# Performance work log

Hardware: AMD Instinct MI355X
Metric: run time of the kernel (lower is better)

Reference implementation:

```python
import jax, jax.numpy as jnp
import numpy as np

DIM = 1024
N_HEADS = 16
HEAD_DIM = DIM // N_HEADS
MLP_DIM = 4096
B, L, M = 4, 1024, 1024
EPS = 1e-5


def _mha(q_in, k_in, v_in, mask, wq, wk, wv, wo):
    b, l, d = q_in.shape
    m = k_in.shape[1]
    # torch view(b, l, head_dim, n_heads): split last dim as (head_dim, n_heads)
    q = (q_in @ wq).reshape(b, l, HEAD_DIM, N_HEADS)
    k = (k_in @ wk).reshape(b, m, HEAD_DIM, N_HEADS)
    v = (v_in @ wv).reshape(b, m, HEAD_DIM, N_HEADS)  # computed but unused downstream (source quirk)
    score = jnp.einsum('bldn,bmdn->blmn', q, k)
    # source applies mask BEFORE scaling
    score = jnp.where(mask, jnp.float32(-1e9), score)
    score = score / (HEAD_DIM ** 0.5)
    attn = jax.nn.softmax(score, axis=2)
    # SOURCE QUIRK: second einsum uses k, not v — reproduced faithfully
    x = jnp.einsum('blmn,bmdn->bldn', attn, k)
    x = x.reshape(b, l, d)  # 'b l d n -> b l (d n)'
    return x @ wo


def _layer_norm(x, g, b):
    mu = jnp.mean(x, axis=-1, keepdims=True)
    var = jnp.var(x, axis=-1, keepdims=True)
    return (x - mu) * jax.lax.rsqrt(var + EPS) * g + b


def setup_inputs() -> dict:
    key = jax.random.key(0)
    ks = jax.random.split(key, 16)
    s = 0.02
    inp = {
        'x': jax.random.normal(ks[0], (B, L, DIM), dtype=jnp.float32),
        'enc_output': jax.random.normal(ks[1], (B, M, DIM), dtype=jnp.float32),
        # causal mask: True above diagonal => masked
        'self_attn_mask': jnp.triu(jnp.ones((L, L), dtype=bool), k=1)[None, :, :, None],
        'enc_dec_mask': jnp.zeros((1, L, M, 1), dtype=bool),
        'sa_wq': s * jax.random.normal(ks[2], (DIM, DIM), jnp.float32),
        'sa_wk': s * jax.random.normal(ks[3], (DIM, DIM), jnp.float32),
        'sa_wv': s * jax.random.normal(ks[4], (DIM, DIM), jnp.float32),
        'sa_wo': s * jax.random.normal(ks[5], (DIM, DIM), jnp.float32),
        'ca_wq': s * jax.random.normal(ks[6], (DIM, DIM), jnp.float32),
        'ca_wk': s * jax.random.normal(ks[7], (DIM, DIM), jnp.float32),
        'ca_wv': s * jax.random.normal(ks[8], (DIM, DIM), jnp.float32),
        'ca_wo': s * jax.random.normal(ks[9], (DIM, DIM), jnp.float32),
        'ln1_g': jnp.ones((DIM,), jnp.float32), 'ln1_b': jnp.zeros((DIM,), jnp.float32),
        'ln2_g': jnp.ones((DIM,), jnp.float32), 'ln2_b': jnp.zeros((DIM,), jnp.float32),
        'ln3_g': jnp.ones((DIM,), jnp.float32), 'ln3_b': jnp.zeros((DIM,), jnp.float32),
        'ff_w1': s * jax.random.normal(ks[10], (DIM, MLP_DIM), jnp.float32),
        'ff_b1': jnp.zeros((MLP_DIM,), jnp.float32),
        'ff_w2': s * jax.random.normal(ks[11], (MLP_DIM, DIM), jnp.float32),
        'ff_b2': jnp.zeros((DIM,), jnp.float32),
    }
    return inp


def reference(x, enc_output, self_attn_mask, enc_dec_mask,
              sa_wq, sa_wk, sa_wv, sa_wo,
              ca_wq, ca_wk, ca_wv, ca_wo,
              ln1_g, ln1_b, ln2_g, ln2_b, ln3_g, ln3_b,
              ff_w1, ff_b1, ff_w2, ff_b2):
    # self-attention + residual + LN (dropout = identity in eval)
    h = x + _mha(x, x, x, self_attn_mask, sa_wq, sa_wk, sa_wv, sa_wo)
    h = _layer_norm(h, ln1_g, ln1_b)
    # encoder-decoder attention + residual + LN
    h = h + _mha(h, enc_output, enc_output, enc_dec_mask, ca_wq, ca_wk, ca_wv, ca_wo)
    h = _layer_norm(h, ln2_g, ln2_b)
    # position-wise FFN (gelu, exact erf like torch default) + residual + LN
    ff = jax.nn.gelu(h @ ff_w1 + ff_b1, approximate=False) @ ff_w2 + ff_b2
    h = h + ff
    h = _layer_norm(h, ln3_g, ln3_b)
    return h
```

## Files before the change

### kernel.cpp

```cpp
#include <hip/hip_runtime.h>
#include <hip/hip_bf16.h>
#include <stdint.h>

typedef unsigned short u16;
typedef _Float16 f16x8 __attribute__((ext_vector_type(8)));
typedef float f32x4 __attribute__((ext_vector_type(4)));

#define TOK 4096

__device__ __forceinline__ u16 f2h(float f) {
  _Float16 h = (_Float16)f;
  return __builtin_bit_cast(unsigned short, h);
}
__device__ __forceinline__ unsigned pack2(float a, float b) {
  return (unsigned)f2h(a) | ((unsigned)f2h(b) << 16);
}
__device__ __forceinline__ void gld16(const u16* g, u16* l) {
  __builtin_amdgcn_global_load_lds(
      (const __attribute__((address_space(1))) void*)g,
      (__attribute__((address_space(3))) void*)l, 16, 0, 0);
}
__device__ __forceinline__ float gelu_fast(float v) {
  float z = 1.5957691216f * v * (1.0f + 0.044715f * v * v);
  return v / (1.0f + __expf(-z));
}

__global__ __launch_bounds__(256) void cast_f16_kernel(const float* __restrict__ in,
                                                       u16* __restrict__ out, int n8) {
  int i = blockIdx.x * 256 + threadIdx.x;
  if (i >= n8) return;
  const float4* p = (const float4*)(in + (size_t)i * 8);
  float4 a = p[0], b = p[1];
  uint4 o;
  o.x = pack2(a.x, a.y); o.y = pack2(a.z, a.w);
  o.z = pack2(b.x, b.y); o.w = pack2(b.z, b.w);
  *(uint4*)(out + (size_t)i * 8) = o;
}

__device__ __forceinline__ void tc_body(const float* W, u16* Wt, int K, int N,
                                        int bx, int by, int tid) {
  __shared__ float tile[32][33];
  int n0 = bx * 32, k0 = by * 32;
  int tx = tid & 31, ty = tid >> 5;
#pragma unroll
  for (int e = 0; e < 4; e++)
    tile[ty + e * 8][tx] = W[(size_t)(k0 + ty + e * 8) * N + n0 + tx];
  __syncthreads();
#pragma unroll
  for (int e = 0; e < 4; e++)
    Wt[(size_t)(n0 + ty + e * 8) * K + k0 + tx] = f2h(tile[tx][ty + e * 8]);
}
__global__ __launch_bounds__(256) void transpose_cast_kernel(const float* __restrict__ W,
                                                             u16* __restrict__ Wt,
                                                             int K, int N) {
  tc_body(W, Wt, K, N, blockIdx.x, blockIdx.y, threadIdx.x);
}
__global__ __launch_bounds__(256) void transpose_cast6_kernel(
    const float* W0, const float* W1, const float* W2,
    const float* W3, const float* W4, const float* W5,
    u16* T0, u16* T1, u16* T2, u16* T3, u16* T4, u16* T5) {
  const float* W; u16* T;
  switch (blockIdx.z) {
    case 0: W = W0; T = T0; break;
    case 1: W = W1; T = T1; break;
    case 2: W = W2; T = T2; break;
    case 3: W = W3; T = T3; break;
    case 4: W = W4; T = T4; break;
    default: W = W5; T = T5; break;
  }
  tc_body(W, T, 1024, 1024, blockIdx.x, blockIdx.y, threadIdx.x);
}

template <int EPI, int BN>
__global__ __launch_bounds__((BN == 256) ? 512 : 256)
void gemm_bt_kernel(const u16* __restrict__ A0,
                    const u16* __restrict__ A1,
                    const u16* __restrict__ Bt0,
                    const u16* __restrict__ Bt1,
                    float* __restrict__ Cf,
                    u16* __restrict__ Cb0,
                    u16* __restrict__ Cb1,
                    u16* __restrict__ CbT,
                    const float* __restrict__ bias,
                    int M, int N, int K, int KLEN) {
  const u16* A  = (EPI == 0 && blockIdx.z) ? A1 : A0;
  const u16* Bt = (EPI == 0 && blockIdx.z) ? Bt1 : Bt0;
  u16* Cb = (EPI == 0 && blockIdx.z) ? Cb1 : Cb0;
  __shared__ u16 As[2][128 * 32];
  __shared__ u16 Bs[2][BN * 32];
  int tid = threadIdx.x, lane = tid & 63, wid = tid >> 6;
  int gx = gridDim.x, gy = gridDim.y;
  int nwg = gx * gy;
  int flat = blockIdx.x + gx * blockIdx.y;
  int k8 = flat & 7, idx = flat >> 3;
  int bx, by;
  if (gx >= 16) {
    int rx = gx >> 2, ry = gy >> 1;
    int kx = k8 & 3, ky = k8 >> 2;
    bx = kx * rx + idx % rx;
    by = ky * ry + idx / rx;
  } else {
    int widx = k8 * (nwg >> 3) + idx;
    bx = widx % gx;
    by = widx / gx;
  }
  int row0 = by * 128, col0 = bx * BN;
  int wm = (BN == 256) ? (wid >> 2) * 64 : (wid >> 1) * 64;
  int wn = (BN == 256) ? (wid & 3) * 64 : (wid & 1) * 64;
  int sr = tid >> 2;
  int scol = (((tid & 3) ^ (sr & 3)) * 8);
  size_t koff = (EPI == 4) ? (size_t)blockIdx.z * KLEN : 0;
  const u16* Ab0 = A + (size_t)(row0 + sr) * K + koff + scol;
  const u16* Ab1 = A + (size_t)(row0 + 64 + sr) * K + koff + scol;
  const u16* Bb0 = Bt + (size_t)(col0 + sr) * K + koff + scol;
  const u16* Bb1 = Bt + (size_t)(col0 + ((BN == 256) ? 128 : 64) + sr) * K + koff + scol;
  f32x4 acc[4][4];
#pragma unroll
  for (int i = 0; i < 4; i++)
#pragma unroll
    for (int j = 0; j < 4; j++) { acc[i][j][0] = 0.f; acc[i][j][1] = 0.f; acc[i][j][2] = 0.f; acc[i][j][3] = 0.f; }
  int KT = KLEN >> 5;
  int ra = lane & 15, kg = lane >> 4;
  int aoff[4], boff[4];
#pragma unroll
  for (int i = 0; i < 4; i++) {
    int r = wm + i * 16 + ra;
    aoff[i] = r * 32 + ((kg ^ (r & 3)) * 8);
    int c = wn + i * 16 + ra;
    boff[i] = c * 32 + ((kg ^ (c & 3)) * 8);
  }

  auto STAGE = [&](int kt, int buf) {
    if constexpr (BN == 256) {
      gld16(Ab0 + kt * 32, &As[buf][wid * 512]);
      gld16(Bb0 + kt * 32, &Bs[buf][wid * 512]);
      gld16(Bb1 + kt * 32, &Bs[buf][4096 + wid * 512]);
    } else {
      gld16(Ab0 + kt * 32, &As[buf][wid * 512]);
      gld16(Ab1 + kt * 32, &As[buf][2048 + wid * 512]);
      gld16(Bb0 + kt * 32, &Bs[buf][wid * 512]);
      gld16(Bb1 + kt * 32, &Bs[buf][2048 + wid * 512]);
    }
  };

  STAGE(0, 0);
  __syncthreads();
  int cur = 0;
  for (int kt = 0; kt < KT; ++kt) {
    if (kt + 1 < KT) STAGE(kt + 1, cur ^ 1);
    f16x8 af[4], bfv[4];
#pragma unroll
    for (int i = 0; i < 4; i++) af[i] = *(const f16x8*)&As[cur][aoff[i]];
#pragma unroll
    for (int j = 0; j < 4; j++) bfv[j] = *(const f16x8*)&Bs[cur][boff[j]];
#pragma unroll
    for (int i = 0; i < 4; i++)
#pragma unroll
      for (int j = 0; j < 4; j++)
        acc[i][j] = __builtin_amdgcn_mfma_f32_16x16x32_f16(af[i], bfv[j], acc[i][j], 0, 0, 0);
    __syncthreads();
    cur ^= 1;
  }

  int rq = kg * 4;
#pragma unroll
  for (int i = 0; i < 4; i++) {
    int rowb = row0 + wm + i * 16 + rq;
    if (EPI == 0) {
      int b = rowb >> 10, l0 = rowb & 1023;
      int d0 = (col0 + wn) >> 4;
      size_t hb = ((size_t)(b * 16 + ra)) * 1024;
      u16 h[4][4];
#pragma unroll
      for (int j = 0; j < 4; j++)
#pragma unroll
        for (int q = 0; q < 4; q++) h[j][q] = f2h(acc[i][j][q]);
#pragma unroll
      for (int q = 0; q < 4; q++) {
        ushort4 hv;
        hv.x = h[0][q]; hv.y = h[1][q]; hv.z = h[2][q]; hv.w = h[3][q];
        *(ushort4*)&Cb[(hb + l0 + q) * 64 + d0] = hv;
      }
      if (blockIdx.z) {
#pragma unroll
        for (int j = 0; j < 4; j++) {
          uint2 ov;
          ov.x = (unsigned)h[j][0] | ((unsigned)h[j][1] << 16);
          ov.y = (unsigned)h[j][2] | ((unsigned)h[j][3] << 16);
          *(uint2*)&CbT[(hb >> 10 << 16) + ((size_t)(d0 + j)) * 1024 + l0] = ov;
        }
      }
    } else {
#pragma unroll
      for (int j = 0; j < 4; j++) {
        int col = col0 + wn + j * 16 + ra;
        float bval = 0.f;
        if (EPI == 2) bval = bias[col];
        if (EPI == 4 && blockIdx.z == 0 && bias) bval = bias[col];
#pragma unroll
        for (int q = 0; q < 4; q++) {
          int row = rowb + q;
          float v = acc[i][j][q] + bval;
          if (EPI == 2) {
            Cb[(size_t)row * N + col] = f2h(gelu_fast(v));
          } else {
            Cf[(size_t)blockIdx.z * M * N + (size_t)row * N + col] = v;
          }
        }
      }
    }
  }
}

template <bool CAUSAL>
__global__ __launch_bounds__(256) void flash3_kernel(const u16* __restrict__ Qh,
                                                     const u16* __restrict__ Kh,
                                                     const u16* __restrict__ KhT,
                                                     u16* __restrict__ Xtok) {
  const int L = 1024;
  int tid = threadIdx.x, lane = tid & 63, wid = tid >> 6;
  int gx = gridDim.x, nwg = gx * gridDim.y;
  int flat = blockIdx.x + gx * blockIdx.y;
  int widx = (flat & 7) * (nwg >> 3) + (flat >> 3);
  int qt = widx % gx, bh = widx / gx;
  if (CAUSAL) qt = gx - 1 - qt;
  __shared__ u16 Ks[2][4096];
  __shared__ u16 Kt[2][4096];
  __shared__ u16 Ps[4][2048];
  int ra = lane & 15, kg = lane >> 4;
  int rq = kg * 4;
  int wr0 = qt * 128 + wid * 32;
  f16x8 qa[2][2];
#pragma unroll
  for (int i = 0; i < 2; i++) {
    const u16* Qb = Qh + ((size_t)bh * L + wr0 + i * 16 + ra) * 64;
    qa[i][0] = *(const f16x8*)(Qb + kg * 8);
    qa[i][1] = *(const f16x8*)(Qb + 32 + kg * 8);
  }
  f32x4 oacc[2][4];
#pragma unroll
  for (int i = 0; i < 2; i++)
#pragma unroll
    for (int d = 0; d < 4; d++) { oacc[i][d][0] = 0.f; oacc[i][d][1] = 0.f; oacc[i][d][2] = 0.f; oacc[i][d][3] = 0.f; }
  float l_i[2][4];
#pragma unroll
  for (int i = 0; i < 2; i++)
#pragma unroll
    for (int q = 0; q < 4; q++) l_i[i][q] = 0.f;
  int ntiles = CAUSAL ? (2 * qt + 2) : 16;
  int fr = lane >> 3, fc = lane & 7;

#define KSTAGE(mt, buf) do {                                                        \
    {                                                                               \
      int rr = wid * 8 + fr;                                                        \
      int cc = fc ^ fr;                                                             \
      gld16(Kh + ((size_t)bh * L + (mt) * 64 + rr) * 64 + cc * 8, &Ks[buf][wid * 512]);          \
      gld16(KhT + ((size_t)bh * 64 + rr) * L + (size_t)(mt) * 64 + cc * 8, &Kt[buf][wid * 512]); \
    }                                                                               \
    {                                                                               \
      int rr = 32 + wid * 8 + fr;                                                   \
      int cc = fc ^ fr;                                                             \
      gld16(Kh + ((size_t)bh * L + (mt) * 64 + rr) * 64 + cc * 8, &Ks[buf][2048 + wid * 512]);          \
      gld16(KhT + ((size_t)bh * 64 + rr) * L + (size_t)(mt) * 64 + cc * 8, &Kt[buf][2048 + wid * 512]); \
    }                                                                               \
  } while (0)

  KSTAGE(0, 0);
  __syncthreads();
  int cur = 0;
  for (int mt = 0; mt < ntiles; ++mt) {
    if (mt + 1 < ntiles) KSTAGE(mt + 1, cur ^ 1);
    bool active = !(CAUSAL && (wr0 + 31 < mt * 64));
    if (active) {
      bool wmask = CAUSAL && (mt * 64 + 63 > wr0);
      float p[2][4][4];
      __builtin_amdgcn_s_setprio(1);
#pragma unroll
      for (int j = 0; j < 4; j++) {
        int krow = j * 16 + ra;
        int s2 = krow & 7;
        f16x8 kb0 = *(const f16x8*)&Ks[cur][krow * 64 + ((kg ^ s2) * 8)];
        f16x8 kb1 = *(const f16x8*)&Ks[cur][krow * 64 + (((4 + kg) ^ s2) * 8)];
#pragma unroll
        for (int i = 0; i < 2; i++) {
          f32x4 a; a[0] = 0.f; a[1] = 0.f; a[2] = 0.f; a[3] = 0.f;
          a = __builtin_amdgcn_mfma_f32_16x16x32_f16(qa[i][0], kb0, a, 0, 0, 0);
          a = __builtin_amdgcn_mfma_f32_16x16x32_f16(qa[i][1], kb1, a, 0, 0, 0);
#pragma unroll
          for (int q = 0; q < 4; q++) {
            float v = a[q] * 0.125f;
            if (wmask) {
              int rg = wr0 + i * 16 + rq + q;
              int cg = mt * 64 + j * 16 + ra;
              if (cg > rg) v = -1.25e8f;
            }
            p[i][j][q] = __expf(v);
          }
        }
      }
      __builtin_amdgcn_s_setprio(0);
#pragma unroll
      for (int i = 0; i < 2; i++) {
        float rs[4] = {0.f, 0.f, 0.f, 0.f};
#pragma unroll
        for (int j = 0; j < 4; j++)
#pragma unroll
          for (int q = 0; q < 4; q++) rs[q] += p[i][j][q];
#pragma unroll
        for (int off = 1; off < 16; off <<= 1)
#pragma unroll
          for (int q = 0; q < 4; q++) rs[q] += __shfl_xor(rs[q], off);
#pragma unroll
        for (int q = 0; q < 4; q++) l_i[i][q] += rs[q];
      }
#pragma unroll
      for (int i = 0; i < 2; i++)
#pragma unroll
        for (int j = 0; j < 4; j++)
#pragma unroll
          for (int q = 0; q < 4; q++) {
            int prow = i * 16 + rq + q;
            int pcol = j * 16 + ra;
            Ps[wid][prow * 64 + (((pcol >> 3) ^ (prow & 7)) * 8) + (pcol & 7)] = f2h(p[i][j][q]);
          }
      f16x8 pa[2][2];
#pragma unroll
      for (int i = 0; i < 2; i++) {
        int arow = i * 16 + ra;
        int s3 = arow & 7;
        pa[i][0] = *(const f16x8*)&Ps[wid][arow * 64 + ((kg ^ s3) * 8)];
        pa[i][1] = *(const f16x8*)&Ps[wid][arow * 64 + (((4 + kg) ^ s3) * 8)];
      }
      __builtin_amdgcn_s_setprio(1);
#pragma unroll
      for (int d = 0; d < 4; d++) {
        int krow = d * 16 + ra;
        int s4 = krow & 7;
        f16x8 kc0 = *(const f16x8*)&Kt[cur][krow * 64 + ((kg ^ s4) * 8)];
        f16x8 kc1 = *(const f16x8*)&Kt[cur][krow * 64 + (((4 + kg) ^ s4) * 8)];
#pragma unroll
        for (int i = 0; i < 2; i++) {
          oacc[i][d] = __builtin_amdgcn_mfma_f32_16x16x32_f16(pa[i][0], kc0, oacc[i][d], 0, 0, 0);
          oacc[i][d] = __builtin_amdgcn_mfma_f32_16x16x32_f16(pa[i][1], kc1, oacc[i][d], 0, 0, 0);
        }
      }
      __builtin_amdgcn_s_setprio(0);
    }
    __syncthreads();
    cur ^= 1;
  }
#undef KSTAGE
  int b = bh >> 4, nh = bh & 15;
#pragma unroll
  for (int i = 0; i < 2; i++)
#pragma unroll
    for (int q = 0; q < 4; q++) {
      float inv = 1.0f / l_i[i][q];
      int l = wr0 + i * 16 + rq + q;
      size_t rowg = ((size_t)b * 1024 + l) * 1024;
#pragma unroll
      for (int d = 0; d < 4; d++)
        Xtok[rowg + (d * 16 + ra) * 16 + nh] = f2h(oacc[i][d][q] * inv);
    }
}

template <int WRITE_H, int TWO>
__global__ __launch_bounds__(256) void ln_kernel(const float* __restrict__ a,
                                                 const float* __restrict__ a2,
                                                 const float* __restrict__ res,
                                                 const float* __restrict__ g,
                                                 const float* __restrict__ bb,
                                                 float* __restrict__ outf,
                                                 u16* __restrict__ outh) {
  int row = blockIdx.x, tid = threadIdx.x;
  int lane = tid & 63, wid = tid >> 6;
  size_t base = (size_t)row * 1024 + tid * 4;
  float4 va = *(const float4*)(a + base);
  float4 vr = *(const float4*)(res + base);
  float x0 = va.x + vr.x, x1 = va.y + vr.y, x2 = va.z + vr.z, x3 = va.w + vr.w;
  if (TWO) {
    float4 v2 = *(const float4*)(a2 + base);
    x0 += v2.x; x1 += v2.y; x2 += v2.z; x3 += v2.w;
  }
  float s = x0 + x1 + x2 + x3;
  float sq = x0 * x0 + x1 * x1 + x2 * x2 + x3 * x3;
#pragma unroll
  for (int off = 1; off < 64; off <<= 1) {
    s += __shfl_xor(s, off);
    sq += __shfl_xor(sq, off);
  }
  __shared__ float red[8];
  if (lane == 0) { red[wid] = s; red[4 + wid] = sq; }
  __syncthreads();
  s = red[0] + red[1] + red[2] + red[3];
  sq = red[4] + red[5] + red[6] + red[7];
  float mean = s * (1.0f / 1024.0f);
  float var = sq * (1.0f / 1024.0f) - mean * mean;
  float rstd = rsqrtf(var + 1e-5f);
  float4 vg = *(const float4*)(g + tid * 4);
  float4 vb = *(const float4*)(bb + tid * 4);
  float y0 = (x0 - mean) * rstd * vg.x + vb.x;
  float y1 = (x1 - mean) * rstd * vg.y + vb.y;
  float y2 = (x2 - mean) * rstd * vg.z + vb.z;
  float y3 = (x3 - mean) * rstd * vg.w + vb.w;
  float4 yo; yo.x = y0; yo.y = y1; yo.z = y2; yo.w = y3;
  *(float4*)(outf + base) = yo;
  if (WRITE_H) {
    uint2 ov; ov.x = pack2(y0, y1); ov.y = pack2(y2, y3);
    *(uint2*)(outh + base) = ov;
  }
}

extern "C" void kernel_launch(void* const* d_in, const int* in_sizes, int n_in,
                              void* d_out, int out_size, void* d_ws, size_t ws_size,
                              hipStream_t stream) {
  (void)in_sizes; (void)n_in; (void)out_size; (void)ws_size;
  const float* x    = (const float*)d_in[0];
  const float* enc  = (const float*)d_in[1];
  const float* sa_wq = (const float*)d_in[4];
  const float* sa_wk = (const float*)d_in[5];
  const float* sa_wo = (const float*)d_in[7];
  const float* ca_wq = (const float*)d_in[8];
  const float* ca_wk = (const float*)d_in[9];
  const float* ca_wo = (const float*)d_in[11];
  const float* ln1g = (const float*)d_in[12];
  const float* ln1b = (const float*)d_in[13];
  const float* ln2g = (const float*)d_in[14];
  const float* ln2b = (const float*)d_in[15];
  const float* ln3g = (const float*)d_in[16];
  const float* ln3b = (const float*)d_in[17];
  const float* ffw1 = (const float*)d_in[18];
  const float* ffb1 = (const float*)d_in[19];
  const float* ffw2 = (const float*)d_in[20];
  const float* ffb2 = (const float*)d_in[21];

  uint8_t* w = (uint8_t*)d_ws;
  const size_t MB = 1024ull * 1024ull;
  u16* wt_saq = (u16*)(w + 0 * MB);
  u16* wt_sak = (u16*)(w + 2 * MB);
  u16* wt_sao = (u16*)(w + 4 * MB);
  u16* wt_caq = (u16*)(w + 6 * MB);
  u16* wt_cak = (u16*)(w + 8 * MB);
  u16* wt_cao = (u16*)(w + 10 * MB);
  u16* wt_ff1 = (u16*)(w + 12 * MB);
  u16* wt_ff2 = (u16*)(w + 20 * MB);
  u16* act_h  = (u16*)(w + 28 * MB);
  u16* enc_h  = (u16*)(w + 36 * MB);
  u16* qhd    = (u16*)(w + 44 * MB);
  u16* khd    = (u16*)(w + 52 * MB);
  u16* khdT   = (u16*)(w + 60 * MB);
  u16* ctxtok = (u16*)(w + 68 * MB);
  float* Cf32 = (float*)(w + 76 * MB);
  float* hA   = (float*)(w + 108 * MB);
  float* hB   = (float*)(w + 124 * MB);
  u16* ff1h = qhd;
  float* Cf32b = Cf32 + 4194304;

  cast_f16_kernel<<<2048, 256, 0, stream>>>(x, act_h, 524288);
  cast_f16_kernel<<<2048, 256, 0, stream>>>(enc, enc_h, 524288);
  transpose_cast6_kernel<<<dim3(32, 32, 6), 256, 0, stream>>>(
      sa_wq, sa_wk, sa_wo, ca_wq, ca_wk, ca_wo,
      wt_saq, wt_sak, wt_sao, wt_caq, wt_cak, wt_cao);
  transpose_cast_kernel<<<dim3(128, 32), 256, 0, stream>>>(ffw1, wt_ff1, 1024, 4096);
  transpose_cast_kernel<<<dim3(32, 128), 256, 0, stream>>>(ffw2, wt_ff2, 4096, 1024);

  gemm_bt_kernel<0, 128><<<dim3(8, 32, 2), 256, 0, stream>>>(
      act_h, act_h, wt_saq, wt_sak, nullptr, qhd, khd, khdT, nullptr, TOK, 1024, 1024, 1024);
  flash3_kernel<true><<<dim3(8, 64), 256, 0, stream>>>(qhd, khd, khdT, ctxtok);
  gemm_bt_kernel<4, 128><<<dim3(8, 32, 2), 256, 0, stream>>>(
      ctxtok, ctxtok, wt_sao, wt_sao, Cf32, nullptr, nullptr, nullptr, nullptr, TOK, 1024, 1024, 512);
  ln_kernel<1, 1><<<4096, 256, 0, stream>>>(Cf32, Cf32b, x, ln1g, ln1b, hA, act_h);

  gemm_bt_kernel<0, 128><<<dim3(8, 32, 2), 256, 0, stream>>>(
      act_h, enc_h, wt_caq, wt_cak, nullptr, qhd, khd, khdT, nullptr, TOK, 1024, 1024, 1024);
  flash3_kernel<false><<<dim3(8, 64), 256, 0, stream>>>(qhd, khd, khdT, ctxtok);
  gemm_bt_kernel<4, 128><<<dim3(8, 32, 2), 256, 0, stream>>>(
      ctxtok, ctxtok, wt_cao, wt_cao, Cf32, nullptr, nullptr, nullptr, nullptr, TOK, 1024, 1024, 512);
  ln_kernel<1, 1><<<4096, 256, 0, stream>>>(Cf32, Cf32b, hA, ln2g, ln2b, hB, act_h);

  gemm_bt_kernel<2, 256><<<dim3(16, 32, 1), 512, 0, stream>>>(
      act_h, act_h, wt_ff1, wt_ff1, nullptr, ff1h, ff1h, nullptr, ffb1, TOK, 4096, 1024, 1024);
  gemm_bt_kernel<4, 128><<<dim3(8, 32, 2), 256, 0, stream>>>(
      ff1h, ff1h, wt_ff2, wt_ff2, Cf32, nullptr, nullptr, nullptr, ffb2, TOK, 1024, 4096, 2048);
  ln_kernel<0, 1><<<4096, 256, 0, stream>>>(Cf32, Cf32b, hB, ln3g, ln3b, (float*)d_out, nullptr);
}
```

Baseline: 370.3 us.

## Store split-K partials in fp16, fuse prep kernels, widen FF2 split-K to four

The split-K GEMM partial outputs are now written as fp16 instead of fp32, and the layer-norm kernel sums a template number of fp16 partials with the residual. This halves partial-sum traffic. The FF2 GEMM moves from two to four K splits for more parallelism. All input casts and weight transposes are merged into one launch. Rounding each partial to fp16 loses some accuracy before the residual add.

After: 362.9 us. 2.0% less time.

```diff
diff --git a/kernel.cpp b/kernel.cpp
--- a/kernel.cpp
+++ b/kernel.cpp
@@ -11,6 +11,9 @@
 __device__ __forceinline__ u16 f2h(float f) {
   _Float16 h = (_Float16)f;
   return __builtin_bit_cast(unsigned short, h);
+}
+__device__ __forceinline__ float h2f(u16 b) {
+  return (float)__builtin_bit_cast(_Float16, b);
 }
 __device__ __forceinline__ unsigned pack2(float a, float b) {
   return (unsigned)f2h(a) | ((unsigned)f2h(b) << 16);
@@ -25,10 +28,21 @@
   return v / (1.0f + __expf(-z));
 }
 
-__global__ __launch_bounds__(256) void cast_f16_kernel(const float* __restrict__ in,
-                                                       u16* __restrict__ out, int n8) {
-  int i = blockIdx.x * 256 + threadIdx.x;
-  if (i >= n8) return;
+__device__ __forceinline__ void tc_body(const float* W, u16* Wt, int K, int N,
+                                        int bx, int by, int tid) {
+  __shared__ float tile[32][33];
+  int n0 = bx * 32, k0 = by * 32;
+  int tx = tid & 31, ty = tid >> 5;
+#pragma unroll
+  for (int e = 0; e < 4; e++)
+    tile[ty + e * 8][tx] = W[(size_t)(k0 + ty + e * 8) * N + n0 + tx];
+  __syncthreads();
+#pragma unroll
+  for (int e = 0; e < 4; e++)
+    Wt[(size_t)(n0 + ty + e * 8) * K + k0 + tx] = f2h(tile[tx][ty + e * 8]);
+}
+__device__ __forceinline__ void cast_body(const float* in, u16* out, int blk, int tid) {
+  int i = blk * 256 + tid;
   const float4* p = (const float4*)(in + (size_t)i * 8);
   float4 a = p[0], b = p[1];
   uint4 o;
@@ -37,38 +51,39 @@
   *(uint4*)(out + (size_t)i * 8) = o;
 }
 
-__device__ __forceinline__ void tc_body(const float* W, u16* Wt, int K, int N,
-                                        int bx, int by, int tid) {
-  __shared__ float tile[32][33];
-  int n0 = bx * 32, k0 = by * 32;
-  int tx = tid & 31, ty = tid >> 5;
-#pragma unroll
-  for (int e = 0; e < 4; e++)
-    tile[ty + e * 8][tx] = W[(size_t)(k0 + ty + e * 8) * N + n0 + tx];
-  __syncthreads();
-#pragma unroll
-  for (int e = 0; e < 4; e++)
-    Wt[(size_t)(n0 + ty + e * 8) * K + k0 + tx] = f2h(tile[tx][ty + e * 8]);
-}
-__global__ __launch_bounds__(256) void transpose_cast_kernel(const float* __restrict__ W,
-                                                             u16* __restrict__ Wt,
-                                                             int K, int N) {
-  tc_body(W, Wt, K, N, blockIdx.x, blockIdx.y, threadIdx.x);
-}
-__global__ __launch_bounds__(256) void transpose_cast6_kernel(
+__global__ __launch_bounds__(256) void prep_kernel(
+    const float* x, const float* enc, u16* xh, u16* ench,
     const float* W0, const float* W1, const float* W2,
     const float* W3, const float* W4, const float* W5,
-    u16* T0, u16* T1, u16* T2, u16* T3, u16* T4, u16* T5) {
-  const float* W; u16* T;
-  switch (blockIdx.z) {
-    case 0: W = W0; T = T0; break;
-    case 1: W = W1; T = T1; break;
-    case 2: W = W2; T = T2; break;
-    case 3: W = W3; T = T3; break;
-    case 4: W = W4; T = T4; break;
-    default: W = W5; T = T5; break;
-  }
-  tc_body(W, T, 1024, 1024, blockIdx.x, blockIdx.y, threadIdx.x);
+    u16* T0, u16* T1, u16* T2, u16* T3, u16* T4, u16* T5,
+    const float* Wff1, u16* Tff1, const float* Wff2, u16* Tff2) {
+  int blk = blockIdx.x, tid = threadIdx.x;
+  if (blk < 2048) { cast_body(x, xh, blk, tid); return; }
+  if (blk < 4096) { cast_body(enc, ench, blk - 2048, tid); return; }
+  if (blk < 10240) {
+    int t = blk - 4096;
+    int z = t >> 10, s = t & 1023;
+    const float* W; u16* T;
+    switch (z) {
+      case 0: W = W0; T = T0; break;
+      case 1: W = W1; T = T1; break;
+      case 2: W = W2; T = T2; break;
+      case 3: W = W3; T = T3; break;
+      case 4: W = W4; T = T4; break;
+      default: W = W5; T = T5; break;
+    }
+    tc_body(W, T, 1024, 1024, s & 31, s >> 5, tid);
+    return;
+  }
+  if (blk < 14336) {
+    int t = blk - 10240;
+    tc_body(Wff1, Tff1, 1024, 4096, t & 127, t >> 7, tid);
+    return;
+  }
+  {
+    int t = blk - 14336;
+    tc_body(Wff2, Tff2, 4096, 1024, t & 31, t >> 5, tid);
+  }
 }
 
 template <int EPI, int BN>
@@ -77,7 +92,6 @@
                     const u16* __restrict__ A1,
                     const u16* __restrict__ Bt0,
                     const u16* __restrict__ Bt1,
-                    float* __restrict__ Cf,
                     u16* __restrict__ Cb0,
                     u16* __restrict__ Cb1,
                     u16* __restrict__ CbT,
@@ -204,7 +218,7 @@
           if (EPI == 2) {
             Cb[(size_t)row * N + col] = f2h(gelu_fast(v));
           } else {
-            Cf[(size_t)blockIdx.z * M * N + (size_t)row * N + col] = v;
+            Cb[(size_t)blockIdx.z * M * N + (size_t)row * N + col] = f2h(v);
           }
         }
       }
@@ -364,9 +378,8 @@
     }
 }
 
-template <int WRITE_H, int TWO>
-__global__ __launch_bounds__(256) void ln_kernel(const float* __restrict__ a,
-                                                 const float* __restrict__ a2,
+template <int WRITE_H, int P>
+__global__ __launch_bounds__(256) void ln_kernel(const u16* __restrict__ parts,
                                                  const float* __restrict__ res,
                                                  const float* __restrict__ g,
                                                  const float* __restrict__ bb,
@@ -375,12 +388,15 @@
   int row = blockIdx.x, tid = threadIdx.x;
   int lane = tid & 63, wid = tid >> 6;
   size_t base = (size_t)row * 1024 + tid * 4;
-  float4 va = *(const float4*)(a + base);
   float4 vr = *(const float4*)(res + base);
-  float x0 = va.x + vr.x, x1 = va.y + vr.y, x2 = va.z + vr.z, x3 = va.w + vr.w;
-  if (TWO) {
-    float4 v2 = *(const float4*)(a2 + base);
-    x0 += v2.x; x1 += v2.y; x2 += v2.z; x3 += v2.w;
+  float x0 = vr.x, x1 = vr.y, x2 = vr.z, x3 = vr.w;
+#pragma unroll
+  for (int p = 0; p < P; p++) {
+    uint2 v = *(const uint2*)&parts[(size_t)p * 4194304 + base];
+    x0 += h2f((u16)v.x);
+    x1 += h2f((u16)(v.x >> 16));
+    x2 += h2f((u16)v.y);
+    x3 += h2f((u16)(v.y >> 16));
   }
   float s = x0 + x1 + x2 + x3;
   float sq = x0 * x0 + x1 * x1 + x2 * x2 + x3 * x3;
@@ -450,37 +466,34 @@
   u16* khd    = (u16*)(w + 52 * MB);
   u16* khdT   = (u16*)(w + 60 * MB);
   u16* ctxtok = (u16*)(w + 68 * MB);
-  float* Cf32 = (float*)(w + 76 * MB);
+  u16* parts  = (u16*)(w + 76 * MB);
   float* hA   = (float*)(w + 108 * MB);
   float* hB   = (float*)(w + 124 * MB);
   u16* ff1h = qhd;
-  float* Cf32b = Cf32 + 4194304;
-
-  cast_f16_kernel<<<2048, 256, 0, stream>>>(x, act_h, 524288);
-  cast_f16_kernel<<<2048, 256, 0, stream>>>(enc, enc_h, 524288);
-  transpose_cast6_kernel<<<dim3(32, 32, 6), 256, 0, stream>>>(
+
+  prep_kernel<<<18432, 256, 0, stream>>>(
+      x, enc, act_h, enc_h,
       sa_wq, sa_wk, sa_wo, ca_wq, ca_wk, ca_wo,
-      wt_saq, wt_sak, wt_sao, wt_caq, wt_cak, wt_cao);
-  transpose_cast_kernel<<<dim3(128, 32), 256, 0, stream>>>(ffw1, wt_ff1, 1024, 4096);
-  transpose_cast_kernel<<<dim3(32, 128), 256, 0, stream>>>(ffw2, wt_ff2, 4096, 1024);
+      wt_saq, wt_sak, wt_sao, wt_caq, wt_cak, wt_cao,
+      ffw1, wt_ff1, ffw2, wt_ff2);
 
   gemm_bt_kernel<0, 128><<<dim3(8, 32, 2), 256, 0, stream>>>(
-      act_h, act_h, wt_saq, wt_sak, nullptr, qhd, khd, khdT, nullptr, TOK, 1024, 1024, 1024);
+      act_h, act_h, wt_saq, wt_sak, qhd, khd, khdT, nullptr, TOK, 1024, 1024, 1024);
   flash3_kernel<true><<<dim3(8, 64), 256, 0, stream>>>(qhd, khd, khdT, ctxtok);
   gemm_bt_kernel<4, 128><<<dim3(8, 32, 2), 256, 0, stream>>>(
-      ctxtok, ctxtok, wt_sao, wt_sao, Cf32, nullptr, nullptr, nullptr, nullptr, TOK, 1024, 1024, 512);
-  ln_kernel<1, 1><<<4096, 256, 0, stream>>>(Cf32, Cf32b, x, ln1g, ln1b, hA, act_h);
+      ctxtok, ctxtok, wt_sao, wt_sao, parts, nullptr, nullptr, nullptr, TOK, 1024, 1024, 512);
+  ln_kernel<1, 2><<<4096, 256, 0, stream>>>(parts, x, ln1g, ln1b, hA, act_h);
 
   gemm_bt_kernel<0, 128><<<dim3(8, 32, 2), 256, 0, stream>>>(
-      act_h, enc_h, wt_caq, wt_cak, nullptr, qhd, khd, khdT, nullptr, TOK, 1024, 1024, 1024);
+      act_h, enc_h, wt_caq, wt_cak, qhd, khd, khdT, nullptr, TOK, 1024, 1024, 1024);
   flash3_kernel<false><<<dim3(8, 64), 256, 0, stream>>>(qhd, khd, khdT, ctxtok);
   gemm_bt_kernel<4, 128><<<dim3(8, 32, 2), 256, 0, stream>>>(
-      ctxtok, ctxtok, wt_cao, wt_cao, Cf32, nullptr, nullptr, nullptr, nullptr, TOK, 1024, 1024, 512);
-  ln_kernel<1, 1><<<4096, 256, 0, stream>>>(Cf32, Cf32b, hA, ln2g, ln2b, hB, act_h);
+      ctxtok, ctxtok, wt_cao, wt_cao, parts, nullptr, nullptr, nullptr, TOK, 1024, 1024, 512);
+  ln_kernel<1, 2><<<4096, 256, 0, stream>>>(parts, hA, ln2g, ln2b, hB, act_h);
 
   gemm_bt_kernel<2, 256><<<dim3(16, 32, 1), 512, 0, stream>>>(
-      act_h, act_h, wt_ff1, wt_ff1, nullptr, ff1h, ff1h, nullptr, ffb1, TOK, 4096, 1024, 1024);
-  gemm_bt_kernel<4, 128><<<dim3(8, 32, 2), 256, 0, stream>>>(
-      ff1h, ff1h, wt_ff2, wt_ff2, Cf32, nullptr, nullptr, nullptr, ffb2, TOK, 1024, 4096, 2048);
-  ln_kernel<0, 1><<<4096, 256, 0, stream>>>(Cf32, Cf32b, hB, ln3g, ln3b, (float*)d_out, nullptr);
-}
+      act_h, act_h, wt_ff1, wt_ff1, ff1h, nullptr, nullptr, ffb1, TOK, 4096, 1024, 1024);
+  gemm_bt_kernel<4, 128><<<dim3(8, 32, 4), 256, 0, stream>>>(
+      ff1h, ff1h, wt_ff2, wt_ff2, parts, nullptr, nullptr, ffb2, TOK, 1024, 4096, 1024);
+  ln_kernel<0, 4><<<4096, 256, 0, stream>>>(parts, hB, ln3g, ln3b, (float*)d_out, nullptr);
+}
```
